# Performance work log

Hardware: AMD Instinct MI355X
Metric: run time of the kernel (lower is better)

## Reference

```python
import jax, jax.numpy as jnp
import numpy as np

N_NODES = 100000


def spmm(edge_src, edge_dst, edge_val, x):
    """z[dst] += val * x[src] over all edges (COO sparse-dense matmul)."""
    gathered = edge_val[:, None] * x[edge_src]  # [E, d]
    return jax.ops.segment_sum(gathered, edge_dst, num_segments=N_NODES)


def setup_inputs() -> dict:
    key = jax.random.key(0)
    k1, k2, k3, k4, k5, k6 = jax.random.split(key, 6)
    N, E, IN, H, C = N_NODES, 1600000, 256, 128, 40
    features = jax.random.normal(k1, (N, IN), dtype=jnp.float32)
    # xavier_uniform-like init
    b1 = float(np.sqrt(6.0 / (IN + H)))
    b2 = float(np.sqrt(6.0 / (H + C)))
    W1 = jax.random.uniform(k2, (IN, H), dtype=jnp.float32, minval=-b1, maxval=b1)
    W2 = jax.random.uniform(k3, (H, C), dtype=jnp.float32, minval=-b2, maxval=b2)
    edge_src = jax.random.randint(k4, (E,), 0, N, dtype=jnp.int32)
    edge_dst = jnp.sort(jax.random.randint(k5, (E,), 0, N, dtype=jnp.int32))
    # normalized-adjacency-like positive edge weights
    edge_val = jax.random.uniform(k6, (E,), dtype=jnp.float32)
    return {"features": features, "W1": W1, "W2": W2,
            "edge_src": edge_src, "edge_dst": edge_dst, "edge_val": edge_val}


def reference(features, W1, W2, edge_src, edge_dst, edge_val):
    # Decoupled GCN: all dense NN layers first (relu between, none after last) ...
    h = jax.nn.relu(features @ W1)
    h = h @ W2  # [N, num_classes]
    # ... then nlayers (=2) rounds of graph propagation (spmm aggregation)
    h = spmm(edge_src, edge_dst, edge_val, h)
    h = spmm(edge_src, edge_dst, edge_val, h)
    return h
```

## Files before the change

kernel.cpp:

```cpp
#include <hip/hip_runtime.h>
#include <cstddef>
#include <cstdint>

#define IN_DIM 256
#define H_DIM  128
#define C_DIM  40
#define BM     128
#define LDH    136
#define PAD_C  40
#define W2_ROWS 64
#define STEP   512
#define RBSLAB 8192

typedef short bf16x8 __attribute__((ext_vector_type(8)));
typedef float f32x16 __attribute__((ext_vector_type(16)));
typedef uint  u32x4  __attribute__((ext_vector_type(4)));

__device__ __forceinline__ ushort f2bf(float f) {
  uint u = __builtin_bit_cast(uint, f);
  u += 0x7fffu + ((u >> 16) & 1u);
  return (ushort)(u >> 16);
}
__device__ __forceinline__ float bf2f(uint s) {
  uint u = s << 16;
  return __builtin_bit_cast(float, u);
}
__device__ __forceinline__ uint pack2bf(float a, float b) {
#if __has_builtin(__builtin_amdgcn_cvt_pk_bf16_f32)
  typedef __bf16 bf16v2 __attribute__((ext_vector_type(2)));
  bf16v2 r = __builtin_amdgcn_cvt_pk_bf16_f32(a, b);
  return __builtin_bit_cast(uint, r);
#else
  return (uint)f2bf(a) | ((uint)f2bf(b) << 16);
#endif
}

__global__ void setup_kernel(const int* __restrict__ dst, int E,
                             int* __restrict__ row_ptr, int n1,
                             const float* __restrict__ W1,
                             const float* __restrict__ W2,
                             const float* __restrict__ feat,
                             ushort* __restrict__ feat_frag,
                             ushort* __restrict__ b_frag,
                             ushort* __restrict__ w2t,
                             int N, int feat_items) {
  int tid = blockIdx.x * blockDim.x + threadIdx.x;
  if (tid < feat_items) {
    int l = tid & 63, ks = (tid >> 6) & 15, rb = tid >> 10;
    int row = rb * 32 + (l & 31); if (row >= N) row = N - 1;
    int col = ks * 16 + ((l >> 5) << 3);
    const float4* p = (const float4*)(feat + (size_t)row * IN_DIM + col);
    float4 v0 = p[0], v1 = p[1];
    uint4 pk;
    pk.x = pack2bf(v0.x, v0.y);
    pk.y = pack2bf(v0.z, v0.w);
    pk.z = pack2bf(v1.x, v1.y);
    pk.w = pack2bf(v1.z, v1.w);
    *(uint4*)(feat_frag + (size_t)tid * 8) = pk;
    return;
  }
  int u = tid - feat_items;
  if (u < 4096) {
    int l = u & 63, ks = (u >> 6) & 15, tn = u >> 10;
    int n  = 32 * tn + (l & 31);
    int k0 = ks * 16 + ((l >> 5) << 3);
    ushort r[8];
#pragma unroll
    for (int j = 0; j < 8; ++j) r[j] = f2bf(W1[(k0 + j) * H_DIM + n]);
    *(uint4*)(b_frag + u * 8) = *(uint4*)r;
    return;
  }
  u -= 4096;
  if (u < W2_ROWS * H_DIM) {
    int n = u >> 7, k = u & 127;
    w2t[u] = (n < C_DIM) ? f2bf(W2[k * C_DIM + n]) : (ushort)0;
    return;
  }
  u -= W2_ROWS * H_DIM;
  if (u < n1) {
    int lo = 0, hi = E;
    while (lo < hi) {
      int mid = (lo + hi) >> 1;
      if (dst[mid] < u) lo = mid + 1; else hi = mid;
    }
    row_ptr[u] = lo;
  }
}

__global__ __launch_bounds__(256, 3) void fused_dense_kernel(
    const ushort* __restrict__ feat_frag, const ushort* __restrict__ b_frag,
    const ushort* __restrict__ w2t, ushort* __restrict__ z0, int N) {
  __shared__ __align__(16) ushort smem[26112];

  const int t = threadIdx.x;
  const int w = t >> 6, l = t & 63;
  const int nb = blockIdx.x * BM;
  const int rb = blockIdx.x * 4 + w;

  f32x16 acc[4];
#pragma unroll
  for (int tn = 0; tn < 4; ++tn)
#pragma unroll
    for (int r = 0; r < 16; ++r) acc[tn][r] = 0.f;

  const ushort* ap = feat_frag + (size_t)rb * RBSLAB + l * 8;
  const ushort* bp = b_frag + l * 8;

  bf16x8 Ax[2];
  bf16x8 Bx[2][4];
  Ax[0] = *(const bf16x8*)(ap);
#pragma unroll
  for (int tn = 0; tn < 4; ++tn)
    Bx[0][tn] = *(const bf16x8*)(bp + tn * (16 * STEP));

#pragma unroll
  for (int ks = 0; ks < 16; ++ks) {
    const int c = ks & 1;
    if (ks < 15) {
      Ax[c ^ 1] = *(const bf16x8*)(ap + (ks + 1) * STEP);
#pragma unroll
      for (int tn = 0; tn < 4; ++tn)
        Bx[c ^ 1][tn] = *(const bf16x8*)(bp + tn * (16 * STEP) + (ks + 1) * STEP);
    }
#pragma unroll
    for (int tn = 0; tn < 4; ++tn)
      acc[tn] = __builtin_amdgcn_mfma_f32_32x32x16_bf16(Ax[c], Bx[c][tn], acc[tn], 0, 0, 0);
  }

#pragma unroll
  for (int tn = 0; tn < 4; ++tn) {
    int col = tn * 32 + (l & 31);
#pragma unroll
    for (int r = 0; r < 16; ++r) {
      int nodeLoc = (r & 3) + 8 * (r >> 2) + 4 * (l >> 5) + 32 * w;
      float v = acc[tn][r];
      smem[nodeLoc * LDH + col] = f2bf(v > 0.f ? v : 0.f);
    }
  }
  {
    int row = t >> 2, c4 = (t & 3) << 5;
    const uint4* src = (const uint4*)(w2t + row * H_DIM + c4);
    uint4* dst = (uint4*)(smem + 128 * LDH + row * LDH + c4);
    dst[0] = src[0];
    dst[1] = src[1];
    dst[2] = src[2];
    dst[3] = src[3];
  }
  __syncthreads();

  f32x16 acc2[2];
#pragma unroll
  for (int tn = 0; tn < 2; ++tn)
#pragma unroll
    for (int r = 0; r < 16; ++r) acc2[tn][r] = 0.f;

  const ushort* Hbase  = smem + (w * 32 + (l & 31)) * LDH + ((l >> 5) << 3);
  const ushort* W2base = smem + 128 * LDH + (l & 31) * LDH + ((l >> 5) << 3);
#pragma unroll
  for (int kb = 0; kb < 8; ++kb) {
    bf16x8 af = *(const bf16x8*)(Hbase + kb * 16);
#pragma unroll
    for (int tn = 0; tn < 2; ++tn) {
      bf16x8 bfr = *(const bf16x8*)(W2base + tn * 32 * LDH + kb * 16);
      acc2[tn] = __builtin_amdgcn_mfma_f32_32x32x16_bf16(af, bfr, acc2[tn], 0, 0, 0);
    }
  }

#pragma unroll
  for (int tn = 0; tn < 2; ++tn) {
    int col = tn * 32 + (l & 31);
    if (col < C_DIM) {
#pragma unroll
      for (int r = 0; r < 16; ++r) {
        int node = nb + 32 * w + (r & 3) + 8 * (r >> 2) + 4 * (l >> 5);
        if (node < N) z0[(size_t)node * PAD_C + col] = f2bf(acc2[tn][r]);
      }
    }
  }
}

__global__ __launch_bounds__(256) void spmm_kernel(
    const int* __restrict__ row_ptr, const int* __restrict__ esrc,
    const float* __restrict__ eval, const ushort* __restrict__ x,
    ushort* __restrict__ zb, float* __restrict__ zf, int N, int out_f32) {
  int node = (blockIdx.x << 2) + (threadIdx.x >> 6);
  if (node >= N) return;
  const int lane = threadIdx.x & 63;
  const int h = lane >> 3;
  const int j = lane & 7;
  const bool act = (j < 5);

  int e   = row_ptr[node];
  int end = row_ptr[node + 1];

  float acc[8];
#pragma unroll
  for (int c = 0; c < 8; ++c) acc[c] = 0.f;

  for (; e + 16 <= end; e += 16) {
    int   s0 = esrc[e + h];
    int   s1 = esrc[e + 8 + h];
    float v0 = eval[e + h];
    float v1 = eval[e + 8 + h];
    if (act) {
      u32x4 a = *(const u32x4*)(x + (size_t)s0 * PAD_C + j * 8);
      u32x4 b = *(const u32x4*)(x + (size_t)s1 * PAD_C + j * 8);
      acc[0] = fmaf(v0, bf2f(a.x & 0xffffu), acc[0]);
      acc[1] = fmaf(v0, bf2f(a.x >> 16),     acc[1]);
      acc[2] = fmaf(v0, bf2f(a.y & 0xffffu), acc[2]);
      acc[3] = fmaf(v0, bf2f(a.y >> 16),     acc[3]);
      acc[4] = fmaf(v0, bf2f(a.z & 0xffffu), acc[4]);
      acc[5] = fmaf(v0, bf2f(a.z >> 16),     acc[5]);
      acc[6] = fmaf(v0, bf2f(a.w & 0xffffu), acc[6]);
      acc[7] = fmaf(v0, bf2f(a.w >> 16),     acc[7]);
      acc[0] = fmaf(v1, bf2f(b.x & 0xffffu), acc[0]);
      acc[1] = fmaf(v1, bf2f(b.x >> 16),     acc[1]);
      acc[2] = fmaf(v1, bf2f(b.y & 0xffffu), acc[2]);
      acc[3] = fmaf(v1, bf2f(b.y >> 16),     acc[3]);
      acc[4] = fmaf(v1, bf2f(b.z & 0xffffu), acc[4]);
      acc[5] = fmaf(v1, bf2f(b.z >> 16),     acc[5]);
      acc[6] = fmaf(v1, bf2f(b.w & 0xffffu), acc[6]);
      acc[7] = fmaf(v1, bf2f(b.w >> 16),     acc[7]);
    }
  }
  for (; e + 8 <= end; e += 8) {
    int   s = esrc[e + h];
    float v = eval[e + h];
    if (act) {
      u32x4 u = *(const u32x4*)(x + (size_t)s * PAD_C + j * 8);
      acc[0] = fmaf(v, bf2f(u.x & 0xffffu), acc[0]);
      acc[1] = fmaf(v, bf2f(u.x >> 16),     acc[1]);
      acc[2] = fmaf(v, bf2f(u.y & 0xffffu), acc[2]);
      acc[3] = fmaf(v, bf2f(u.y >> 16),     acc[3]);
      acc[4] = fmaf(v, bf2f(u.z & 0xffffu), acc[4]);
      acc[5] = fmaf(v, bf2f(u.z >> 16),     acc[5]);
      acc[6] = fmaf(v, bf2f(u.w & 0xffffu), acc[6]);
      acc[7] = fmaf(v, bf2f(u.w >> 16),     acc[7]);
    }
  }
  if (e < end) {
    int ei = e + h;
    int ec = ei < end ? ei : end - 1;
    int   s  = esrc[ec];
    float v0 = eval[ec];
    float v  = ei < end ? v0 : 0.f;
    if (act) {
      u32x4 u = *(const u32x4*)(x + (size_t)s * PAD_C + j * 8);
      acc[0] = fmaf(v, bf2f(u.x & 0xffffu), acc[0]);
      acc[1] = fmaf(v, bf2f(u.x >> 16),     acc[1]);
      acc[2] = fmaf(v, bf2f(u.y & 0xffffu), acc[2]);
      acc[3] = fmaf(v, bf2f(u.y >> 16),     acc[3]);
      acc[4] = fmaf(v, bf2f(u.z & 0xffffu), acc[4]);
      acc[5] = fmaf(v, bf2f(u.z >> 16),     acc[5]);
      acc[6] = fmaf(v, bf2f(u.w & 0xffffu), acc[6]);
      acc[7] = fmaf(v, bf2f(u.w >> 16),     acc[7]);
    }
  }

#pragma unroll
  for (int c = 0; c < 8; ++c) acc[c] += __shfl_xor(acc[c], 8);
#pragma unroll
  for (int c = 0; c < 8; ++c) acc[c] += __shfl_xor(acc[c], 16);
#pragma unroll
  for (int c = 0; c < 8; ++c) acc[c] += __shfl_xor(acc[c], 32);

  if (out_f32) {
    if (lane < 5) {
      float4 o0 = {acc[0], acc[1], acc[2], acc[3]};
      float4 o1 = {acc[4], acc[5], acc[6], acc[7]};
      float* p = zf + (size_t)node * C_DIM + j * 8;
      *(float4*)(p + 0) = o0;
      *(float4*)(p + 4) = o1;
    }
  } else {
    if (lane < 5) {
      uint4 p;
      p.x = (uint)f2bf(acc[0]) | ((uint)f2bf(acc[1]) << 16);
      p.y = (uint)f2bf(acc[2]) | ((uint)f2bf(acc[3]) << 16);
      p.z = (uint)f2bf(acc[4]) | ((uint)f2bf(acc[5]) << 16);
      p.w = (uint)f2bf(acc[6]) | ((uint)f2bf(acc[7]) << 16);
      *(uint4*)(zb + (size_t)node * PAD_C + j * 8) = p;
    }
  }
}

extern "C" void kernel_launch(void* const* d_in, const int* in_sizes, int n_in,
                              void* d_out, int out_size, void* d_ws, size_t ws_size,
                              hipStream_t stream) {
  const float* feat  = (const float*)d_in[0];
  const float* W1    = (const float*)d_in[1];
  const float* W2    = (const float*)d_in[2];
  const int*   esrc  = (const int*)d_in[3];
  const int*   edst  = (const int*)d_in[4];
  const float* evalp = (const float*)d_in[5];
  float* out = (float*)d_out;

  const int N = in_sizes[0] / IN_DIM;
  const int E = in_sizes[3];

  const int nblk  = (N + BM - 1) / BM;
  const int rbmax = nblk * 4;
  const int feat_items = rbmax * 1024;

  char* ws = (char*)d_ws;
  ushort* z0        = (ushort*)ws;
  ushort* z1        = (ushort*)(ws + (size_t)N * PAD_C * 2);
  ushort* feat_frag = (ushort*)(ws + (size_t)N * PAD_C * 4);
  ushort* b_frag    = feat_frag + (size_t)rbmax * RBSLAB;
  ushort* w2t       = b_frag + 4 * 16 * STEP;
  int* row_ptr      = (int*)(w2t + W2_ROWS * H_DIM);

  const int setup_items = feat_items + 4096 + W2_ROWS * H_DIM + (N + 1);
  setup_kernel<<<(setup_items + 255) / 256, 256, 0, stream>>>(
      edst, E, row_ptr, N + 1, W1, W2, feat, feat_frag, b_frag, w2t, N, feat_items);
  fused_dense_kernel<<<nblk, 256, 0, stream>>>(feat_frag, b_frag, w2t, z0, N);
  spmm_kernel<<<(N + 3) / 4, 256, 0, stream>>>(row_ptr, esrc, evalp, z0, z1, nullptr, N, 0);
  spmm_kernel<<<(N + 3) / 4, 256, 0, stream>>>(row_ptr, esrc, evalp, z1, nullptr, out, N, 1);
}
```

Measured before the change: 290.5 us.

## Fuse feature bf16 conversion into dense kernel via LDS; build row_ptr by edge scan

The separate pass that converted features to bf16 MFMA fragments in global memory is removed. The dense kernel now loads fp32 feature rows directly, converts them to bf16 and stages them in a padded LDS tile, cutting a full write and re-read of the feature matrix. Row pointers are built by each edge thread writing boundaries from adjacent sorted dst values, replacing per-node binary searches. LDS use grows to about 66KB and occupancy drops to 2 blocks per CU. Row_ptr filling is uneven where there are long gaps in dst.

```diff
diff --git a/kernel.cpp b/kernel.cpp
--- a/kernel.cpp
+++ b/kernel.cpp
@@ -6,11 +6,11 @@
 #define H_DIM  128
 #define C_DIM  40
 #define BM     128
+#define LDA    264
 #define LDH    136
 #define PAD_C  40
 #define W2_ROWS 64
 #define STEP   512
-#define RBSLAB 8192
 
 typedef short bf16x8 __attribute__((ext_vector_type(8)));
 typedef float f32x16 __attribute__((ext_vector_type(16)));
@@ -36,30 +36,21 @@
 }
 
 __global__ void setup_kernel(const int* __restrict__ dst, int E,
-                             int* __restrict__ row_ptr, int n1,
+                             int* __restrict__ row_ptr, int N,
                              const float* __restrict__ W1,
                              const float* __restrict__ W2,
-                             const float* __restrict__ feat,
-                             ushort* __restrict__ feat_frag,
                              ushort* __restrict__ b_frag,
-                             ushort* __restrict__ w2t,
-                             int N, int feat_items) {
+                             ushort* __restrict__ w2t) {
   int tid = blockIdx.x * blockDim.x + threadIdx.x;
-  if (tid < feat_items) {
-    int l = tid & 63, ks = (tid >> 6) & 15, rb = tid >> 10;
-    int row = rb * 32 + (l & 31); if (row >= N) row = N - 1;
-    int col = ks * 16 + ((l >> 5) << 3);
-    const float4* p = (const float4*)(feat + (size_t)row * IN_DIM + col);
-    float4 v0 = p[0], v1 = p[1];
-    uint4 pk;
-    pk.x = pack2bf(v0.x, v0.y);
-    pk.y = pack2bf(v0.z, v0.w);
-    pk.z = pack2bf(v1.x, v1.y);
-    pk.w = pack2bf(v1.z, v1.w);
-    *(uint4*)(feat_frag + (size_t)tid * 8) = pk;
+  if (tid < E) {
+    int d1 = dst[tid];
+    int d0 = (tid == 0) ? -1 : dst[tid - 1];
+    for (int v = d0 + 1; v <= d1; ++v) row_ptr[v] = tid;
+    if (tid == E - 1)
+      for (int v = d1 + 1; v <= N; ++v) row_ptr[v] = E;
     return;
   }
-  int u = tid - feat_items;
+  int u = tid - E;
   if (u < 4096) {
     int l = u & 63, ks = (u >> 6) & 15, tn = u >> 10;
     int n  = 32 * tn + (l & 31);
@@ -74,28 +65,17 @@
   if (u < W2_ROWS * H_DIM) {
     int n = u >> 7, k = u & 127;
     w2t[u] = (n < C_DIM) ? f2bf(W2[k * C_DIM + n]) : (ushort)0;
-    return;
-  }
-  u -= W2_ROWS * H_DIM;
-  if (u < n1) {
-    int lo = 0, hi = E;
-    while (lo < hi) {
-      int mid = (lo + hi) >> 1;
-      if (dst[mid] < u) lo = mid + 1; else hi = mid;
-    }
-    row_ptr[u] = lo;
-  }
-}
-
-__global__ __launch_bounds__(256, 3) void fused_dense_kernel(
-    const ushort* __restrict__ feat_frag, const ushort* __restrict__ b_frag,
+  }
+}
+
+__global__ __launch_bounds__(256, 2) void fused_dense_kernel(
+    const float* __restrict__ feat, const ushort* __restrict__ b_frag,
     const ushort* __restrict__ w2t, ushort* __restrict__ z0, int N) {
-  __shared__ __align__(16) ushort smem[26112];
+  __shared__ __align__(16) ushort smem[128 * LDA];
 
   const int t = threadIdx.x;
   const int w = t >> 6, l = t & 63;
   const int nb = blockIdx.x * BM;
-  const int rb = blockIdx.x * 4 + w;
 
   f32x16 acc[4];
 #pragma unroll
@@ -103,29 +83,39 @@
 #pragma unroll
     for (int r = 0; r < 16; ++r) acc[tn][r] = 0.f;
 
-  const ushort* ap = feat_frag + (size_t)rb * RBSLAB + l * 8;
   const ushort* bp = b_frag + l * 8;
-
-  bf16x8 Ax[2];
   bf16x8 Bx[2][4];
-  Ax[0] = *(const bf16x8*)(ap);
 #pragma unroll
   for (int tn = 0; tn < 4; ++tn)
     Bx[0][tn] = *(const bf16x8*)(bp + tn * (16 * STEP));
 
+#pragma unroll
+  for (int c = 0; c < 32; ++c) {
+    int row = 4 * c + w;
+    int grow = nb + row; if (grow >= N) grow = N - 1;
+    float4 v = *(const float4*)(feat + (size_t)grow * IN_DIM + l * 4);
+    uint2 pk;
+    pk.x = pack2bf(v.x, v.y);
+    pk.y = pack2bf(v.z, v.w);
+    *(uint2*)(smem + row * LDA + l * 4) = pk;
+  }
+  __syncthreads();
+
+  const ushort* Abase = smem + (w * 32 + (l & 31)) * LDA + ((l >> 5) << 3);
 #pragma unroll
   for (int ks = 0; ks < 16; ++ks) {
     const int c = ks & 1;
     if (ks < 15) {
-      Ax[c ^ 1] = *(const bf16x8*)(ap + (ks + 1) * STEP);
 #pragma unroll
       for (int tn = 0; tn < 4; ++tn)
         Bx[c ^ 1][tn] = *(const bf16x8*)(bp + tn * (16 * STEP) + (ks + 1) * STEP);
     }
+    bf16x8 af = *(const bf16x8*)(Abase + ks * 16);
 #pragma unroll
     for (int tn = 0; tn < 4; ++tn)
-      acc[tn] = __builtin_amdgcn_mfma_f32_32x32x16_bf16(Ax[c], Bx[c][tn], acc[tn], 0, 0, 0);
-  }
+      acc[tn] = __builtin_amdgcn_mfma_f32_32x32x16_bf16(af, Bx[c][tn], acc[tn], 0, 0, 0);
+  }
+  __syncthreads();
 
 #pragma unroll
   for (int tn = 0; tn < 4; ++tn) {
@@ -298,22 +288,19 @@
   const int N = in_sizes[0] / IN_DIM;
   const int E = in_sizes[3];
 
-  const int nblk  = (N + BM - 1) / BM;
-  const int rbmax = nblk * 4;
-  const int feat_items = rbmax * 1024;
+  const int nblk = (N + BM - 1) / BM;
 
   char* ws = (char*)d_ws;
-  ushort* z0        = (ushort*)ws;
-  ushort* z1        = (ushort*)(ws + (size_t)N * PAD_C * 2);
-  ushort* feat_frag = (ushort*)(ws + (size_t)N * PAD_C * 4);
-  ushort* b_frag    = feat_frag + (size_t)rbmax * RBSLAB;
-  ushort* w2t       = b_frag + 4 * 16 * STEP;
-  int* row_ptr      = (int*)(w2t + W2_ROWS * H_DIM);
-
-  const int setup_items = feat_items + 4096 + W2_ROWS * H_DIM + (N + 1);
+  ushort* z0     = (ushort*)ws;
+  ushort* z1     = (ushort*)(ws + (size_t)N * PAD_C * 2);
+  ushort* b_frag = (ushort*)(ws + (size_t)N * PAD_C * 4);
+  ushort* w2t    = b_frag + 4 * 16 * STEP;
+  int* row_ptr   = (int*)(w2t + W2_ROWS * H_DIM);
+
+  const int setup_items = E + 4096 + W2_ROWS * H_DIM;
   setup_kernel<<<(setup_items + 255) / 256, 256, 0, stream>>>(
-      edst, E, row_ptr, N + 1, W1, W2, feat, feat_frag, b_frag, w2t, N, feat_items);
-  fused_dense_kernel<<<nblk, 256, 0, stream>>>(feat_frag, b_frag, w2t, z0, N);
+      edst, E, row_ptr, N, W1, W2, b_frag, w2t);
+  fused_dense_kernel<<<nblk, 256, 0, stream>>>(feat, b_frag, w2t, z0, N);
   spmm_kernel<<<(N + 3) / 4, 256, 0, stream>>>(row_ptr, esrc, evalp, z0, z1, nullptr, N, 0);
   spmm_kernel<<<(N + 3) / 4, 256, 0, stream>>>(row_ptr, esrc, evalp, z1, nullptr, out, N, 1);
 }
```

Result: faster. 275.3 us (-5.2%).
